# Kernel optimization log

Hardware: AMD Instinct MI355X
Metric: run time of the kernel (lower is better)

## Reference

```python
import jax, jax.numpy as jnp
import numpy as np

B, S, DH, EH, A = 32, 4096, 512, 512, 256

def setup_inputs() -> dict:
    key = jax.random.key(0)
    k1, k2, k3, k4, k5, k6 = jax.random.split(key, 6)
    decoder_hidden = jax.random.normal(k1, (B, DH), dtype=jnp.float32)
    encoder_outputs = jax.random.normal(k2, (B, S, EH), dtype=jnp.float32)
    mask = jax.random.randint(k3, (B, S), 0, 2, dtype=jnp.int32)
    # torch Linear(in, out, bias=False) weight is (out, in); store transposed (in, out)
    Wd = jax.random.normal(k4, (DH, A), dtype=jnp.float32) * (1.0 / np.sqrt(DH))
    We = jax.random.normal(k5, (EH, A), dtype=jnp.float32) * (1.0 / np.sqrt(EH))
    v = jax.random.normal(k6, (A,), dtype=jnp.float32) * (1.0 / np.sqrt(A))
    return {"decoder_hidden": decoder_hidden, "encoder_outputs": encoder_outputs,
            "mask": mask, "Wd": Wd, "We": We, "v": v}

def reference(decoder_hidden, encoder_outputs, mask, Wd, We, v):
    # score = v^T tanh(Wd h_t + We h_s)  -- broadcast decoder proj over src_len
    dec_proj = decoder_hidden @ Wd                      # (B, A)
    enc_proj = jnp.einsum('bse,ea->bsa', encoder_outputs, We)  # (B, S, A)
    energy = jnp.tanh(dec_proj[:, None, :] + enc_proj) @ v     # (B, S)
    energy = jnp.where(mask == 0, -jnp.inf, energy)
    attn = jax.nn.softmax(energy, axis=-1)
    attn = jnp.nan_to_num(attn, nan=0.0)
    context = jnp.einsum('bs,bse->be', attn, encoder_outputs)  # (B, EH)
    return (context, attn)
```

## Files before the change

### kernel.cpp

```cpp
#include <hip/hip_runtime.h>
#include <hip/hip_bf16.h>
#include <math.h>

#define BB 32
#define SS 4096
#define DHH 512
#define EHH 512
#define AA 256

typedef __attribute__((ext_vector_type(8))) short bf16x8;
typedef __attribute__((ext_vector_type(4))) float f32x4;

__device__ __forceinline__ short f2bf(float f) {
    unsigned u = __float_as_uint(f);
    u += 0x7FFFu + ((u >> 16) & 1u);
    return (short)(u >> 16);
}

__device__ __forceinline__ unsigned cvt2bf(float a, float b) {
    __hip_bfloat162 h = __float22bfloat162_rn(float2{a, b});
    return *(unsigned*)&h;
}

__device__ __forceinline__ float tanh_fast(float x) {
    float e = __expf(2.0f * x);
    return 1.0f - 2.0f * __builtin_amdgcn_rcpf(e + 1.0f);
}

__global__ __launch_bounds__(256) void k_packWe(const float* __restrict__ We,
                                                unsigned short* __restrict__ Wpack) {
    int tid = threadIdx.x;
    int e = blockIdx.x * 4 + (tid >> 6);
    int a4 = (tid & 63) * 4;
    float4 t = *(const float4*)&We[(size_t)e * AA + a4];
    int kk = e >> 5, hi = (e >> 3) & 3, j = e & 7;
    const float* tf = (const float*)&t;
    #pragma unroll
    for (int u = 0; u < 4; ++u) {
        int a = a4 + u;
        int ct = a >> 4, lo = a & 15;
        Wpack[((size_t)((kk * 16 + ct) * 64 + hi * 16 + lo)) * 8 + j] = (unsigned short)f2bf(tf[u]);
    }
}

__global__ __launch_bounds__(256) void k_decproj(const float* __restrict__ h,
                                                 const float* __restrict__ Wd,
                                                 float* __restrict__ dp8) {
    int b = blockIdx.x, sp = blockIdx.y;
    int a = threadIdx.x;
    const float* hb = h + (size_t)b * DHH + sp * 64;
    const float* wb = Wd + (size_t)(sp * 64) * AA + a;
    float acc = 0.f;
    #pragma unroll 16
    for (int i = 0; i < 64; ++i)
        acc = fmaf(hb[i], wb[(size_t)i * AA], acc);
    dp8[((size_t)b * 8 + sp) * AA + a] = acc;
}

__global__ __launch_bounds__(256, 4) void k_energy_mfma(const float* __restrict__ enc,
                                                        const unsigned short* __restrict__ Wpack,
                                                        const float* __restrict__ dp8,
                                                        const float* __restrict__ v,
                                                        const int* __restrict__ mask,
                                                        float* __restrict__ energy,
                                                        float* __restrict__ pctx,
                                                        float2* __restrict__ ml) {
    __shared__ unsigned short Abuf[8][32 * 64];
    __shared__ float part[4][32];
    __shared__ float wbuf[32];

    int bk = blockIdx.x;
    int b  = bk >> 7;
    int chunk = bk & 127;
    int s0 = chunk * 32;
    int tid = threadIdx.x;
    int l  = tid & 63;
    int w  = tid >> 6;
    int lo = l & 15;
    int hi = l >> 4;

    int r = tid >> 3;
    int q = tid & 7;
    const float* gbase = enc + ((size_t)b * SS + s0 + r) * EHH + q * 8;
    int wb0 = ((r * 128 + q * 16) ^ ((r & 7) << 4));

    float4 sva[8], svb[8];
    #pragma unroll
    for (int kt = 0; kt < 8; ++kt) {
        const float4* gp = (const float4*)(gbase + kt * 64);
        sva[kt] = gp[0]; svb[kt] = gp[1];
    }
    #pragma unroll
    for (int kt = 0; kt < 8; ++kt) {
        uint4 w0 = { cvt2bf(sva[kt].x, sva[kt].y), cvt2bf(sva[kt].z, sva[kt].w),
                     cvt2bf(svb[kt].x, svb[kt].y), cvt2bf(svb[kt].z, svb[kt].w) };
        *(uint4*)((char*)Abuf[kt] + wb0) = w0;
    }
    __syncthreads();

    f32x4 acc[2][4];
    #pragma unroll
    for (int rt = 0; rt < 2; ++rt)
        #pragma unroll
        for (int ct = 0; ct < 4; ++ct)
            acc[rt][ct] = (f32x4){0.f, 0.f, 0.f, 0.f};

    const unsigned short* bbase = Wpack + ((size_t)(w * 4) * 64 + l) * 8;
    bf16x8 bn0[4], bn1[4];
    #pragma unroll
    for (int ct = 0; ct < 4; ++ct) bn0[ct] = *(const bf16x8*)(bbase + ct * 512);
    #pragma unroll
    for (int ct = 0; ct < 4; ++ct) bn1[ct] = *(const bf16x8*)(bbase + 8192 + ct * 512);

    #pragma unroll
    for (int g = 0; g < 16; ++g) {
        int kt = g >> 1, ks = g & 1;
        bf16x8 bcur[4];
        #pragma unroll
        for (int ct = 0; ct < 4; ++ct) { bcur[ct] = bn0[ct]; bn0[ct] = bn1[ct]; }
        if (g + 2 < 16) {
            const unsigned short* bp = bbase + (size_t)(g + 2) * 8192;
            #pragma unroll
            for (int ct = 0; ct < 4; ++ct)
                bn1[ct] = *(const bf16x8*)(bp + ct * 512);
        }
        const char* lb = (const char*)Abuf[kt];
        bf16x8 afr[2];
        #pragma unroll
        for (int rt = 0; rt < 2; ++rt) {
            int row = rt * 16 + lo;
            afr[rt] = *(const bf16x8*)(lb + ((row * 128 + ks * 64 + hi * 16) ^ ((row & 7) << 4)));
        }
        #pragma unroll
        for (int rt = 0; rt < 2; ++rt)
            #pragma unroll
            for (int ct = 0; ct < 4; ++ct)
                acc[rt][ct] = __builtin_amdgcn_mfma_f32_16x16x32_bf16(afr[rt], bcur[ct], acc[rt][ct], 0, 0, 0);
    }

    float ps[2][4];
    #pragma unroll
    for (int rt = 0; rt < 2; ++rt)
        #pragma unroll
        for (int rr = 0; rr < 4; ++rr) ps[rt][rr] = 0.f;
    #pragma unroll
    for (int ct = 0; ct < 4; ++ct) {
        int n = w * 64 + ct * 16 + lo;
        float dpv = 0.f;
        #pragma unroll
        for (int sp = 0; sp < 8; ++sp)
            dpv += dp8[((size_t)b * 8 + sp) * AA + n];
        float vv = v[n];
        #pragma unroll
        for (int rt = 0; rt < 2; ++rt)
            #pragma unroll
            for (int rr = 0; rr < 4; ++rr)
                ps[rt][rr] += vv * tanh_fast(acc[rt][ct][rr] + dpv);
    }
    #pragma unroll
    for (int off = 1; off < 16; off <<= 1)
        #pragma unroll
        for (int rt = 0; rt < 2; ++rt)
            #pragma unroll
            for (int rr = 0; rr < 4; ++rr)
                ps[rt][rr] += __shfl_xor(ps[rt][rr], off);
    if (lo == 0) {
        #pragma unroll
        for (int rt = 0; rt < 2; ++rt)
            #pragma unroll
            for (int rr = 0; rr < 4; ++rr)
                part[w][rt * 16 + 4 * hi + rr] = ps[rt][rr];
    }
    __syncthreads();

    if (w == 0 && l < 32) {
        float e = part[0][l] + part[1][l] + part[2][l] + part[3][l];
        energy[(size_t)b * SS + s0 + l] = e;
        int mk = mask[(size_t)b * SS + s0 + l];
        float val = mk ? e : -INFINITY;
        float m = val;
        #pragma unroll
        for (int off = 1; off < 32; off <<= 1) m = fmaxf(m, __shfl_xor(m, off));
        float wgt = (val == -INFINITY) ? 0.f : __expf(val - m);
        float lsum = wgt;
        #pragma unroll
        for (int off = 1; off < 32; off <<= 1) lsum += __shfl_xor(lsum, off);
        wbuf[l] = wgt;
        if (l == 0) ml[(size_t)b * 128 + chunk] = float2{m, lsum};
    }
    __syncthreads();

    {
        int e0 = tid * 2;
        int reg = e0 >> 6;
        int c   = e0 & 63;
        const char* lb = (const char*)Abuf[reg];
        float a0 = 0.f, a1 = 0.f;
        #pragma unroll 8
        for (int s = 0; s < 32; ++s) {
            float wv_ = wbuf[s];
            unsigned u = *(const unsigned*)(lb + ((s * 128 + c * 2) ^ ((s & 7) << 4)));
            float x0 = __uint_as_float(u << 16);
            float x1 = __uint_as_float(u & 0xFFFF0000u);
            a0 = fmaf(wv_, x0, a0);
            a1 = fmaf(wv_, x1, a1);
        }
        *(float2*)&pctx[((size_t)(b * 128 + chunk)) * 512 + e0] = float2{a0, a1};
    }
}

__global__ __launch_bounds__(512) void k_final(const float* __restrict__ energy,
                                               const int* __restrict__ mask,
                                               const float2* __restrict__ ml,
                                               const float* __restrict__ pctx,
                                               float* __restrict__ attn,
                                               float* __restrict__ ctx) {
    __shared__ float wm[8], wz[8];
    __shared__ float red[4][128];
    int b = blockIdx.x, sl = blockIdx.y;
    int tid = threadIdx.x;
    int l = tid & 63, w = tid >> 6;

    float2 p = float2{-INFINITY, 0.f};
    if (tid < 128) p = ml[(size_t)b * 128 + tid];
    float m = p.x;
    #pragma unroll
    for (int off = 1; off < 64; off <<= 1) m = fmaxf(m, __shfl_xor(m, off));
    if (!l) wm[w] = m;
    __syncthreads();
    float M = wm[0];
    #pragma unroll
    for (int i = 1; i < 8; ++i) M = fmaxf(M, wm[i]);
    float z = (p.x == -INFINITY) ? 0.f : __expf(p.x - M) * p.y;
    #pragma unroll
    for (int off = 1; off < 64; off <<= 1) z += __shfl_xor(z, off);
    if (!l) wz[w] = z;
    __syncthreads();
    float Z = 0.f;
    #pragma unroll
    for (int i = 0; i < 8; ++i) Z += wz[i];
    float invZ = (Z > 0.f) ? 1.0f / Z : 0.f;

    #pragma unroll
    for (int it = 0; it < 2; ++it) {
        int s = sl * 1024 + it * 512 + tid;
        float e = energy[(size_t)b * SS + s];
        int mk = mask[(size_t)b * SS + s];
        attn[(size_t)b * SS + s] = mk ? __expf(e - M) * invZ : 0.f;
    }

    {
        int cg = tid >> 7;
        int e  = sl * 128 + (tid & 127);
        float acc = 0.f;
        #pragma unroll 8
        for (int i = 0; i < 32; ++i) {
            int c = cg * 32 + i;
            float2 pc = ml[(size_t)b * 128 + c];
            float sc = (pc.x == -INFINITY) ? 0.f : __expf(pc.x - M);
            acc = fmaf(sc, pctx[((size_t)(b * 128 + c)) * 512 + e], acc);
        }
        red[cg][tid & 127] = acc;
    }
    __syncthreads();
    if (tid < 128) {
        float s = red[0][tid] + red[1][tid] + red[2][tid] + red[3][tid];
        ctx[(size_t)b * EHH + sl * 128 + tid] = s * invZ;
    }
}

extern "C" void kernel_launch(void* const* d_in, const int* in_sizes, int n_in,
                              void* d_out, int out_size, void* d_ws, size_t ws_size,
                              hipStream_t stream) {
    const float* h    = (const float*)d_in[0];
    const float* enc  = (const float*)d_in[1];
    const int*   mask = (const int*)d_in[2];
    const float* Wd   = (const float*)d_in[3];
    const float* We   = (const float*)d_in[4];
    const float* v    = (const float*)d_in[5];

    float* out  = (float*)d_out;
    float* ctx  = out;
    float* attn = out + BB * EHH;

    char* ws = (char*)d_ws;
    float*          dp8    = (float*)ws;
    float*          energy = (float*)(ws + (256 << 10));
    unsigned short* Wpack  = (unsigned short*)(ws + (768 << 10));
    float*          pctx   = (float*)(ws + (1 << 20));
    float2*         ml     = (float2*)(ws + (9 << 20));

    k_packWe<<<128, 256, 0, stream>>>(We, Wpack);
    k_decproj<<<dim3(BB, 8), AA, 0, stream>>>(h, Wd, dp8);
    k_energy_mfma<<<BB * SS / 32, 256, 0, stream>>>(enc, Wpack, dp8, v, mask,
                                                    energy, pctx, ml);
    k_final<<<dim3(BB, 4), 512, 0, stream>>>(energy, mask, ml, pctx, attn, ctx);
}
```

Before: 95.66 us.

## Double energy-kernel tile to 64 rows with 512 threads and halve partial contexts

The energy kernel now handles 64 source positions per block with 8 waves. Each wave computes a 64x32 output slice instead of 32x64, which halves the per-row reads of the packed We fragments. The number of per-chunk partial contexts and (max, sum) pairs drops from 128 to 64 per batch row. This lightens the pctx write/read traffic and simplifies k_final, which now precomputes the chunk scales once in shared memory. In exchange, the block uses 64 KB of LDS, which limits blocks per CU, and the context pass now does scalar 16-bit LDS reads.

```diff
diff --git a/kernel.cpp b/kernel.cpp
--- a/kernel.cpp
+++ b/kernel.cpp
@@ -57,7 +57,7 @@
     dp8[((size_t)b * 8 + sp) * AA + a] = acc;
 }
 
-__global__ __launch_bounds__(256, 4) void k_energy_mfma(const float* __restrict__ enc,
+__global__ __launch_bounds__(512, 4) void k_energy_mfma(const float* __restrict__ enc,
                                                         const unsigned short* __restrict__ Wpack,
                                                         const float* __restrict__ dp8,
                                                         const float* __restrict__ v,
@@ -65,14 +65,14 @@
                                                         float* __restrict__ energy,
                                                         float* __restrict__ pctx,
                                                         float2* __restrict__ ml) {
-    __shared__ unsigned short Abuf[8][32 * 64];
-    __shared__ float part[4][32];
-    __shared__ float wbuf[32];
+    __shared__ unsigned short Abuf[8][64 * 64];
+    __shared__ float part[8][64];
+    __shared__ float wbuf[64];
 
     int bk = blockIdx.x;
-    int b  = bk >> 7;
-    int chunk = bk & 127;
-    int s0 = chunk * 32;
+    int b  = bk >> 6;
+    int chunk = bk & 63;
+    int s0 = chunk * 64;
     int tid = threadIdx.x;
     int l  = tid & 63;
     int w  = tid >> 6;
@@ -98,61 +98,61 @@
     }
     __syncthreads();
 
-    f32x4 acc[2][4];
-    #pragma unroll
-    for (int rt = 0; rt < 2; ++rt)
-        #pragma unroll
-        for (int ct = 0; ct < 4; ++ct)
+    f32x4 acc[4][2];
+    #pragma unroll
+    for (int rt = 0; rt < 4; ++rt)
+        #pragma unroll
+        for (int ct = 0; ct < 2; ++ct)
             acc[rt][ct] = (f32x4){0.f, 0.f, 0.f, 0.f};
 
-    const unsigned short* bbase = Wpack + ((size_t)(w * 4) * 64 + l) * 8;
-    bf16x8 bn0[4], bn1[4];
-    #pragma unroll
-    for (int ct = 0; ct < 4; ++ct) bn0[ct] = *(const bf16x8*)(bbase + ct * 512);
-    #pragma unroll
-    for (int ct = 0; ct < 4; ++ct) bn1[ct] = *(const bf16x8*)(bbase + 8192 + ct * 512);
+    const unsigned short* bbase = Wpack + ((size_t)(w * 2) * 64 + l) * 8;
+    bf16x8 bn0[2], bn1[2];
+    #pragma unroll
+    for (int ct = 0; ct < 2; ++ct) bn0[ct] = *(const bf16x8*)(bbase + ct * 512);
+    #pragma unroll
+    for (int ct = 0; ct < 2; ++ct) bn1[ct] = *(const bf16x8*)(bbase + 8192 + ct * 512);
 
     #pragma unroll
     for (int g = 0; g < 16; ++g) {
         int kt = g >> 1, ks = g & 1;
-        bf16x8 bcur[4];
-        #pragma unroll
-        for (int ct = 0; ct < 4; ++ct) { bcur[ct] = bn0[ct]; bn0[ct] = bn1[ct]; }
+        bf16x8 bcur[2];
+        #pragma unroll
+        for (int ct = 0; ct < 2; ++ct) { bcur[ct] = bn0[ct]; bn0[ct] = bn1[ct]; }
         if (g + 2 < 16) {
             const unsigned short* bp = bbase + (size_t)(g + 2) * 8192;
             #pragma unroll
-            for (int ct = 0; ct < 4; ++ct)
+            for (int ct = 0; ct < 2; ++ct)
                 bn1[ct] = *(const bf16x8*)(bp + ct * 512);
         }
         const char* lb = (const char*)Abuf[kt];
-        bf16x8 afr[2];
-        #pragma unroll
-        for (int rt = 0; rt < 2; ++rt) {
+        bf16x8 afr[4];
+        #pragma unroll
+        for (int rt = 0; rt < 4; ++rt) {
             int row = rt * 16 + lo;
             afr[rt] = *(const bf16x8*)(lb + ((row * 128 + ks * 64 + hi * 16) ^ ((row & 7) << 4)));
         }
         #pragma unroll
-        for (int rt = 0; rt < 2; ++rt)
-            #pragma unroll
-            for (int ct = 0; ct < 4; ++ct)
+        for (int rt = 0; rt < 4; ++rt)
+            #pragma unroll
+            for (int ct = 0; ct < 2; ++ct)
                 acc[rt][ct] = __builtin_amdgcn_mfma_f32_16x16x32_bf16(afr[rt], bcur[ct], acc[rt][ct], 0, 0, 0);
     }
 
-    float ps[2][4];
-    #pragma unroll
-    for (int rt = 0; rt < 2; ++rt)
+    float ps[4][4];
+    #pragma unroll
+    for (int rt = 0; rt < 4; ++rt)
         #pragma unroll
         for (int rr = 0; rr < 4; ++rr) ps[rt][rr] = 0.f;
     #pragma unroll
-    for (int ct = 0; ct < 4; ++ct) {
-        int n = w * 64 + ct * 16 + lo;
+    for (int ct = 0; ct < 2; ++ct) {
+        int n = w * 32 + ct * 16 + lo;
         float dpv = 0.f;
         #pragma unroll
         for (int sp = 0; sp < 8; ++sp)
             dpv += dp8[((size_t)b * 8 + sp) * AA + n];
         float vv = v[n];
         #pragma unroll
-        for (int rt = 0; rt < 2; ++rt)
+        for (int rt = 0; rt < 4; ++rt)
             #pragma unroll
             for (int rr = 0; rr < 4; ++rr)
                 ps[rt][rr] += vv * tanh_fast(acc[rt][ct][rr] + dpv);
@@ -160,52 +160,51 @@
     #pragma unroll
     for (int off = 1; off < 16; off <<= 1)
         #pragma unroll
-        for (int rt = 0; rt < 2; ++rt)
+        for (int rt = 0; rt < 4; ++rt)
             #pragma unroll
             for (int rr = 0; rr < 4; ++rr)
                 ps[rt][rr] += __shfl_xor(ps[rt][rr], off);
     if (lo == 0) {
         #pragma unroll
-        for (int rt = 0; rt < 2; ++rt)
+        for (int rt = 0; rt < 4; ++rt)
             #pragma unroll
             for (int rr = 0; rr < 4; ++rr)
                 part[w][rt * 16 + 4 * hi + rr] = ps[rt][rr];
     }
     __syncthreads();
 
-    if (w == 0 && l < 32) {
-        float e = part[0][l] + part[1][l] + part[2][l] + part[3][l];
+    if (w == 0) {
+        float e = 0.f;
+        #pragma unroll
+        for (int i = 0; i < 8; ++i) e += part[i][l];
         energy[(size_t)b * SS + s0 + l] = e;
         int mk = mask[(size_t)b * SS + s0 + l];
         float val = mk ? e : -INFINITY;
         float m = val;
         #pragma unroll
-        for (int off = 1; off < 32; off <<= 1) m = fmaxf(m, __shfl_xor(m, off));
+        for (int off = 1; off < 64; off <<= 1) m = fmaxf(m, __shfl_xor(m, off));
         float wgt = (val == -INFINITY) ? 0.f : __expf(val - m);
         float lsum = wgt;
         #pragma unroll
-        for (int off = 1; off < 32; off <<= 1) lsum += __shfl_xor(lsum, off);
+        for (int off = 1; off < 64; off <<= 1) lsum += __shfl_xor(lsum, off);
         wbuf[l] = wgt;
-        if (l == 0) ml[(size_t)b * 128 + chunk] = float2{m, lsum};
+        if (l == 0) ml[(size_t)b * 64 + chunk] = float2{m, lsum};
     }
     __syncthreads();
 
     {
-        int e0 = tid * 2;
-        int reg = e0 >> 6;
-        int c   = e0 & 63;
+        int e = tid;
+        int reg = e >> 6;
+        int c2 = (e & 63) * 2;
         const char* lb = (const char*)Abuf[reg];
-        float a0 = 0.f, a1 = 0.f;
+        float a0 = 0.f;
         #pragma unroll 8
-        for (int s = 0; s < 32; ++s) {
+        for (int s = 0; s < 64; ++s) {
             float wv_ = wbuf[s];
-            unsigned u = *(const unsigned*)(lb + ((s * 128 + c * 2) ^ ((s & 7) << 4)));
-            float x0 = __uint_as_float(u << 16);
-            float x1 = __uint_as_float(u & 0xFFFF0000u);
-            a0 = fmaf(wv_, x0, a0);
-            a1 = fmaf(wv_, x1, a1);
-        }
-        *(float2*)&pctx[((size_t)(b * 128 + chunk)) * 512 + e0] = float2{a0, a1};
+            unsigned short u = *(const unsigned short*)(lb + ((s * 128 + c2) ^ ((s & 7) << 4)));
+            a0 = fmaf(wv_, __uint_as_float(((unsigned)u) << 16), a0);
+        }
+        pctx[((size_t)(b * 64 + chunk)) * 512 + e] = a0;
     }
 }
 
@@ -215,31 +214,27 @@
                                                const float* __restrict__ pctx,
                                                float* __restrict__ attn,
                                                float* __restrict__ ctx) {
-    __shared__ float wm[8], wz[8];
+    __shared__ float scal[64];
+    __shared__ float sM, sZ;
     __shared__ float red[4][128];
     int b = blockIdx.x, sl = blockIdx.y;
     int tid = threadIdx.x;
-    int l = tid & 63, w = tid >> 6;
-
-    float2 p = float2{-INFINITY, 0.f};
-    if (tid < 128) p = ml[(size_t)b * 128 + tid];
-    float m = p.x;
-    #pragma unroll
-    for (int off = 1; off < 64; off <<= 1) m = fmaxf(m, __shfl_xor(m, off));
-    if (!l) wm[w] = m;
-    __syncthreads();
-    float M = wm[0];
-    #pragma unroll
-    for (int i = 1; i < 8; ++i) M = fmaxf(M, wm[i]);
-    float z = (p.x == -INFINITY) ? 0.f : __expf(p.x - M) * p.y;
-    #pragma unroll
-    for (int off = 1; off < 64; off <<= 1) z += __shfl_xor(z, off);
-    if (!l) wz[w] = z;
-    __syncthreads();
-    float Z = 0.f;
-    #pragma unroll
-    for (int i = 0; i < 8; ++i) Z += wz[i];
-    float invZ = (Z > 0.f) ? 1.0f / Z : 0.f;
+
+    if (tid < 64) {
+        float2 p = ml[(size_t)b * 64 + tid];
+        float m = p.x;
+        #pragma unroll
+        for (int off = 1; off < 64; off <<= 1) m = fmaxf(m, __shfl_xor(m, off));
+        float sc = (p.x == -INFINITY) ? 0.f : __expf(p.x - m);
+        scal[tid] = sc;
+        float z = sc * p.y;
+        #pragma unroll
+        for (int off = 1; off < 64; off <<= 1) z += __shfl_xor(z, off);
+        if (tid == 0) { sM = m; sZ = z; }
+    }
+    __syncthreads();
+    float M = sM;
+    float invZ = (sZ > 0.f) ? 1.0f / sZ : 0.f;
 
     #pragma unroll
     for (int it = 0; it < 2; ++it) {
@@ -254,11 +249,9 @@
         int e  = sl * 128 + (tid & 127);
         float acc = 0.f;
         #pragma unroll 8
-        for (int i = 0; i < 32; ++i) {
-            int c = cg * 32 + i;
-            float2 pc = ml[(size_t)b * 128 + c];
-            float sc = (pc.x == -INFINITY) ? 0.f : __expf(pc.x - M);
-            acc = fmaf(sc, pctx[((size_t)(b * 128 + c)) * 512 + e], acc);
+        for (int i = 0; i < 16; ++i) {
+            int c = cg * 16 + i;
+            acc = fmaf(scal[c], pctx[((size_t)(b * 64 + c)) * 512 + e], acc);
         }
         red[cg][tid & 127] = acc;
     }
@@ -288,11 +281,11 @@
     float*          energy = (float*)(ws + (256 << 10));
     unsigned short* Wpack  = (unsigned short*)(ws + (768 << 10));
     float*          pctx   = (float*)(ws + (1 << 20));
-    float2*         ml     = (float2*)(ws + (9 << 20));
+    float2*         ml     = (float2*)(ws + (6 << 20));
 
     k_packWe<<<128, 256, 0, stream>>>(We, Wpack);
     k_decproj<<<dim3(BB, 8), AA, 0, stream>>>(h, Wd, dp8);
-    k_energy_mfma<<<BB * SS / 32, 256, 0, stream>>>(enc, Wpack, dp8, v, mask,
+    k_energy_mfma<<<BB * SS / 64, 512, 0, stream>>>(enc, Wpack, dp8, v, mask,
                                                     energy, pctx, ml);
     k_final<<<dim3(BB, 4), 512, 0, stream>>>(energy, mask, ml, pctx, attn, ctx);
 }
```

New measurement: 95.07 us. About the same (-0.6%).

## Make energy kernel persistent over 8 chunks with double-buffered LDS prefetch

Applied to the files above, without the earlier changes.

The energy kernel now launches 512 blocks of 512 threads instead of 4096 blocks of 256. Each block loops over 8 consecutive 32-row chunks and ping-pongs between two LDS buffers, so the global loads for the next chunk overlap the MFMA, tanh and context work on the current one. Each of the 8 waves now covers 32 attention columns instead of 64. The dp/v sums are hoisted out of the chunk loop and the wbuf shared array is replaced by shuffles. The risks are lower block-level parallelism on the device, more LDS per block, and re-reading the We fragments from global or L2 for every chunk.

```diff
diff --git a/kernel.cpp b/kernel.cpp
--- a/kernel.cpp
+++ b/kernel.cpp
@@ -57,126 +57,145 @@
     dp8[((size_t)b * 8 + sp) * AA + a] = acc;
 }
 
-__global__ __launch_bounds__(256, 4) void k_energy_mfma(const float* __restrict__ enc,
-                                                        const unsigned short* __restrict__ Wpack,
-                                                        const float* __restrict__ dp8,
-                                                        const float* __restrict__ v,
-                                                        const int* __restrict__ mask,
-                                                        float* __restrict__ energy,
-                                                        float* __restrict__ pctx,
-                                                        float2* __restrict__ ml) {
-    __shared__ unsigned short Abuf[8][32 * 64];
-    __shared__ float part[4][32];
-    __shared__ float wbuf[32];
-
-    int bk = blockIdx.x;
-    int b  = bk >> 7;
-    int chunk = bk & 127;
-    int s0 = chunk * 32;
+__global__ __launch_bounds__(512) void k_energy_mfma(const float* __restrict__ enc,
+                                                     const unsigned short* __restrict__ Wpack,
+                                                     const float* __restrict__ dp8,
+                                                     const float* __restrict__ v,
+                                                     const int* __restrict__ mask,
+                                                     float* __restrict__ energy,
+                                                     float* __restrict__ pctx,
+                                                     float2* __restrict__ ml) {
+    __shared__ unsigned short AbufA[8][32 * 64];
+    __shared__ unsigned short AbufB[8][32 * 64];
+    __shared__ float part[8][32];
+
+    int slot = blockIdx.x;
+    int b  = slot >> 4;
+    int c0 = (slot & 15) * 8;
     int tid = threadIdx.x;
     int l  = tid & 63;
     int w  = tid >> 6;
     int lo = l & 15;
     int hi = l >> 4;
 
-    int r = tid >> 3;
-    int q = tid & 7;
-    const float* gbase = enc + ((size_t)b * SS + s0 + r) * EHH + q * 8;
-    int wb0 = ((r * 128 + q * 16) ^ ((r & 7) << 4));
-
-    float4 sva[8], svb[8];
-    #pragma unroll
-    for (int kt = 0; kt < 8; ++kt) {
-        const float4* gp = (const float4*)(gbase + kt * 64);
-        sva[kt] = gp[0]; svb[kt] = gp[1];
-    }
-    #pragma unroll
-    for (int kt = 0; kt < 8; ++kt) {
-        uint4 w0 = { cvt2bf(sva[kt].x, sva[kt].y), cvt2bf(sva[kt].z, sva[kt].w),
-                     cvt2bf(svb[kt].x, svb[kt].y), cvt2bf(svb[kt].z, svb[kt].w) };
-        *(uint4*)((char*)Abuf[kt] + wb0) = w0;
+    int r = tid >> 4;
+    int q = tid & 15;
+    const float* gb0 = enc + ((size_t)(b * SS + c0 * 32 + r)) * EHH + q * 32;
+    int ktw = q >> 1, half = q & 1;
+    int wo[4];
+    #pragma unroll
+    for (int i = 0; i < 4; ++i)
+        wo[i] = ktw * 4096 + ((r * 128 + half * 64 + i * 16) ^ ((r & 7) << 4));
+
+    float dpv[2], vv[2];
+    #pragma unroll
+    for (int ct = 0; ct < 2; ++ct) {
+        int n = w * 32 + ct * 16 + lo;
+        float d = 0.f;
+        #pragma unroll
+        for (int sp = 0; sp < 8; ++sp)
+            d += dp8[((size_t)b * 8 + sp) * AA + n];
+        dpv[ct] = d;
+        vv[ct]  = v[n];
+    }
+
+    const unsigned short* bbase = Wpack + ((size_t)(w * 2) * 64 + l) * 8;
+
+    float4 st[8];
+    #pragma unroll
+    for (int i = 0; i < 8; ++i) st[i] = *(const float4*)(gb0 + i * 4);
+    unsigned short* bufc = &AbufA[0][0];
+    unsigned short* bufn = &AbufB[0][0];
+    #pragma unroll
+    for (int i = 0; i < 4; ++i) {
+        uint4 wv = { cvt2bf(st[2*i].x, st[2*i].y),   cvt2bf(st[2*i].z, st[2*i].w),
+                     cvt2bf(st[2*i+1].x, st[2*i+1].y), cvt2bf(st[2*i+1].z, st[2*i+1].w) };
+        *(uint4*)((char*)bufc + wo[i]) = wv;
     }
     __syncthreads();
 
-    f32x4 acc[2][4];
-    #pragma unroll
-    for (int rt = 0; rt < 2; ++rt)
-        #pragma unroll
-        for (int ct = 0; ct < 4; ++ct)
-            acc[rt][ct] = (f32x4){0.f, 0.f, 0.f, 0.f};
-
-    const unsigned short* bbase = Wpack + ((size_t)(w * 4) * 64 + l) * 8;
-    bf16x8 bn0[4], bn1[4];
-    #pragma unroll
-    for (int ct = 0; ct < 4; ++ct) bn0[ct] = *(const bf16x8*)(bbase + ct * 512);
-    #pragma unroll
-    for (int ct = 0; ct < 4; ++ct) bn1[ct] = *(const bf16x8*)(bbase + 8192 + ct * 512);
-
-    #pragma unroll
-    for (int g = 0; g < 16; ++g) {
-        int kt = g >> 1, ks = g & 1;
-        bf16x8 bcur[4];
-        #pragma unroll
-        for (int ct = 0; ct < 4; ++ct) { bcur[ct] = bn0[ct]; bn0[ct] = bn1[ct]; }
-        if (g + 2 < 16) {
-            const unsigned short* bp = bbase + (size_t)(g + 2) * 8192;
-            #pragma unroll
-            for (int ct = 0; ct < 4; ++ct)
-                bn1[ct] = *(const bf16x8*)(bp + ct * 512);
-        }
-        const char* lb = (const char*)Abuf[kt];
-        bf16x8 afr[2];
-        #pragma unroll
-        for (int rt = 0; rt < 2; ++rt) {
-            int row = rt * 16 + lo;
-            afr[rt] = *(const bf16x8*)(lb + ((row * 128 + ks * 64 + hi * 16) ^ ((row & 7) << 4)));
-        }
+    for (int c = 0; c < 8; ++c) {
+        int cg = c0 + c;
+        int s0 = cg * 32;
+
+        if (c < 7) {
+            const float* gb = gb0 + (size_t)(c + 1) * 32 * EHH;
+            #pragma unroll
+            for (int i = 0; i < 8; ++i) st[i] = *(const float4*)(gb + i * 4);
+        }
+
+        f32x4 acc[2][2];
         #pragma unroll
         for (int rt = 0; rt < 2; ++rt)
             #pragma unroll
-            for (int ct = 0; ct < 4; ++ct)
-                acc[rt][ct] = __builtin_amdgcn_mfma_f32_16x16x32_bf16(afr[rt], bcur[ct], acc[rt][ct], 0, 0, 0);
-    }
-
-    float ps[2][4];
-    #pragma unroll
-    for (int rt = 0; rt < 2; ++rt)
-        #pragma unroll
-        for (int rr = 0; rr < 4; ++rr) ps[rt][rr] = 0.f;
-    #pragma unroll
-    for (int ct = 0; ct < 4; ++ct) {
-        int n = w * 64 + ct * 16 + lo;
-        float dpv = 0.f;
-        #pragma unroll
-        for (int sp = 0; sp < 8; ++sp)
-            dpv += dp8[((size_t)b * 8 + sp) * AA + n];
-        float vv = v[n];
+            for (int ct = 0; ct < 2; ++ct)
+                acc[rt][ct] = (f32x4){0.f, 0.f, 0.f, 0.f};
+
+        bf16x8 bn0[2], bn1[2];
+        #pragma unroll
+        for (int ct = 0; ct < 2; ++ct) bn0[ct] = *(const bf16x8*)(bbase + ct * 512);
+        #pragma unroll
+        for (int ct = 0; ct < 2; ++ct) bn1[ct] = *(const bf16x8*)(bbase + 8192 + ct * 512);
+
+        #pragma unroll
+        for (int g = 0; g < 16; ++g) {
+            int kt = g >> 1, ks = g & 1;
+            bf16x8 bcur[2];
+            #pragma unroll
+            for (int ct = 0; ct < 2; ++ct) { bcur[ct] = bn0[ct]; bn0[ct] = bn1[ct]; }
+            if (g + 2 < 16) {
+                const unsigned short* bp = bbase + (size_t)(g + 2) * 8192;
+                #pragma unroll
+                for (int ct = 0; ct < 2; ++ct)
+                    bn1[ct] = *(const bf16x8*)(bp + ct * 512);
+            }
+            bf16x8 afr[2];
+            #pragma unroll
+            for (int rt = 0; rt < 2; ++rt) {
+                int row = rt * 16 + lo;
+                afr[rt] = *(const bf16x8*)((char*)bufc + kt * 4096
+                           + ((row * 128 + ks * 64 + hi * 16) ^ ((row & 7) << 4)));
+            }
+            #pragma unroll
+            for (int rt = 0; rt < 2; ++rt)
+                #pragma unroll
+                for (int ct = 0; ct < 2; ++ct)
+                    acc[rt][ct] = __builtin_amdgcn_mfma_f32_16x16x32_bf16(afr[rt], bcur[ct], acc[rt][ct], 0, 0, 0);
+        }
+
+        float ps[2][4];
         #pragma unroll
         for (int rt = 0; rt < 2; ++rt)
             #pragma unroll
-            for (int rr = 0; rr < 4; ++rr)
-                ps[rt][rr] += vv * tanh_fast(acc[rt][ct][rr] + dpv);
-    }
-    #pragma unroll
-    for (int off = 1; off < 16; off <<= 1)
-        #pragma unroll
-        for (int rt = 0; rt < 2; ++rt)
-            #pragma unroll
-            for (int rr = 0; rr < 4; ++rr)
-                ps[rt][rr] += __shfl_xor(ps[rt][rr], off);
-    if (lo == 0) {
-        #pragma unroll
-        for (int rt = 0; rt < 2; ++rt)
-            #pragma unroll
-            for (int rr = 0; rr < 4; ++rr)
-                part[w][rt * 16 + 4 * hi + rr] = ps[rt][rr];
-    }
-    __syncthreads();
-
-    if (w == 0 && l < 32) {
-        float e = part[0][l] + part[1][l] + part[2][l] + part[3][l];
-        energy[(size_t)b * SS + s0 + l] = e;
-        int mk = mask[(size_t)b * SS + s0 + l];
+            for (int rr = 0; rr < 4; ++rr) ps[rt][rr] = 0.f;
+        #pragma unroll
+        for (int ct = 0; ct < 2; ++ct)
+            #pragma unroll
+            for (int rt = 0; rt < 2; ++rt)
+                #pragma unroll
+                for (int rr = 0; rr < 4; ++rr)
+                    ps[rt][rr] += vv[ct] * tanh_fast(acc[rt][ct][rr] + dpv[ct]);
+        #pragma unroll
+        for (int off = 1; off < 16; off <<= 1)
+            #pragma unroll
+            for (int rt = 0; rt < 2; ++rt)
+                #pragma unroll
+                for (int rr = 0; rr < 4; ++rr)
+                    ps[rt][rr] += __shfl_xor(ps[rt][rr], off);
+        if (lo == 0) {
+            #pragma unroll
+            for (int rt = 0; rt < 2; ++rt)
+                #pragma unroll
+                for (int rr = 0; rr < 4; ++rr)
+                    part[w][rt * 16 + 4 * hi + rr] = ps[rt][rr];
+        }
+        __syncthreads();
+
+        float e = 0.f;
+        #pragma unroll
+        for (int i = 0; i < 8; ++i) e += part[i][l & 31];
+        if (w == 0 && l < 32) energy[(size_t)b * SS + s0 + l] = e;
+        int mk = mask[(size_t)b * SS + s0 + (l & 31)];
         float val = mk ? e : -INFINITY;
         float m = val;
         #pragma unroll
@@ -185,27 +204,32 @@
         float lsum = wgt;
         #pragma unroll
         for (int off = 1; off < 32; off <<= 1) lsum += __shfl_xor(lsum, off);
-        wbuf[l] = wgt;
-        if (l == 0) ml[(size_t)b * 128 + chunk] = float2{m, lsum};
-    }
-    __syncthreads();
-
-    {
-        int e0 = tid * 2;
-        int reg = e0 >> 6;
-        int c   = e0 & 63;
-        const char* lb = (const char*)Abuf[reg];
-        float a0 = 0.f, a1 = 0.f;
-        #pragma unroll 8
-        for (int s = 0; s < 32; ++s) {
-            float wv_ = wbuf[s];
-            unsigned u = *(const unsigned*)(lb + ((s * 128 + c * 2) ^ ((s & 7) << 4)));
-            float x0 = __uint_as_float(u << 16);
-            float x1 = __uint_as_float(u & 0xFFFF0000u);
-            a0 = fmaf(wv_, x0, a0);
-            a1 = fmaf(wv_, x1, a1);
-        }
-        *(float2*)&pctx[((size_t)(b * 128 + chunk)) * 512 + e0] = float2{a0, a1};
+        if (w == 0 && l == 0) ml[(size_t)b * 128 + cg] = float2{m, lsum};
+
+        {
+            int ktp = tid >> 6;
+            int c2  = (tid & 63) * 2;
+            float a0 = 0.f;
+            #pragma unroll 8
+            for (int s = 0; s < 32; ++s) {
+                float wv_ = __shfl(wgt, s);
+                unsigned short u = *(const unsigned short*)((char*)bufc + ktp * 4096
+                                    + ((s * 128 + c2) ^ ((s & 7) << 4)));
+                a0 = fmaf(wv_, __uint_as_float(((unsigned)u) << 16), a0);
+            }
+            pctx[((size_t)(b * 128 + cg)) * 512 + tid] = a0;
+        }
+
+        if (c < 7) {
+            #pragma unroll
+            for (int i = 0; i < 4; ++i) {
+                uint4 wv = { cvt2bf(st[2*i].x, st[2*i].y),   cvt2bf(st[2*i].z, st[2*i].w),
+                             cvt2bf(st[2*i+1].x, st[2*i+1].y), cvt2bf(st[2*i+1].z, st[2*i+1].w) };
+                *(uint4*)((char*)bufn + wo[i]) = wv;
+            }
+        }
+        __syncthreads();
+        unsigned short* t = bufc; bufc = bufn; bufn = t;
     }
 }
 
@@ -292,7 +316,7 @@
 
     k_packWe<<<128, 256, 0, stream>>>(We, Wpack);
     k_decproj<<<dim3(BB, 8), AA, 0, stream>>>(h, Wd, dp8);
-    k_energy_mfma<<<BB * SS / 32, 256, 0, stream>>>(enc, Wpack, dp8, v, mask,
-                                                    energy, pctx, ml);
+    k_energy_mfma<<<BB * 16, 512, 0, stream>>>(enc, Wpack, dp8, v, mask,
+                                               energy, pctx, ml);
     k_final<<<dim3(BB, 4), 512, 0, stream>>>(energy, mask, ml, pctx, attn, ctx);
 }
```

After: 137.1 us. 1.43x slower.
